# Performance work log

Hardware: AMD Instinct MI355X
Metric: run time of the kernel (lower is better)

## Reference

```python
import jax, jax.numpy as jnp
import numpy as np

NUM_ROUTING = 3


def squash(s, axis):
    # v = |s|^2/(1+|s|^2) * s/|s|  (eq. 1 of the CapsNet paper)
    mag_sq = jnp.sum(s * s, axis=axis, keepdims=True)
    mag = jnp.sqrt(mag_sq)
    return mag_sq / (1.0 + mag_sq) * (s / mag)


def setup_inputs() -> dict:
    key = jax.random.key(0)
    k1, k2 = jax.random.split(key)
    B, I, C, U, S = 256, 8, 1152, 10, 16
    x = jax.random.normal(k1, (B, I, C), dtype=jnp.float32)
    weight = jax.random.normal(k2, (1, C, U, S, I), dtype=jnp.float32)
    return {"x": x, "weight": weight}


def reference(x, weight):
    # x: [B, in_unit, in_channel]; weight: [1, C, U, S, I]
    B = x.shape[0]
    C, U = weight.shape[1], weight.shape[2]
    x_t = jnp.transpose(x, (0, 2, 1))  # [B, C, I]
    # u_hat[b,c,u,s] = sum_i W[0,c,u,s,i] * x_t[b,c,i]
    u_hat = jnp.einsum('cusi,bci->bcus', weight[0], x_t)  # [B, C, U, S]

    b_ij = jnp.zeros((1, C, U, 1), dtype=u_hat.dtype)
    # s_j = (c_ij * u_hat).sum(dim=0): c_ij is batch-independent, so
    # precompute the batch-sum once instead of re-broadcasting each iter.
    u_sum = jnp.sum(u_hat, axis=0, keepdims=True)  # [1, C, U, S]

    v_j = None
    for _ in range(NUM_ROUTING):
        c_ij = jax.nn.softmax(b_ij, axis=2)          # [1, C, U, 1]
        s_j = c_ij * u_sum                           # [1, C, U, S]
        v_j = squash(s_j, axis=3)                    # [1, C, U, S]
        # agreement: mean over batch of <u_hat[b,c,u,:], v_j[0,c,u,:]>
        u_vj1 = jnp.einsum('bcus,cus->cu', u_hat, v_j[0]) / B  # [C, U]
        b_ij = b_ij + u_vj1[None, :, :, None]
    return v_j[0]  # squeeze -> [C, U, S]
```

## Files before the change

### kernel.cpp

```cpp
#include <hip/hip_runtime.h>

#define B_DIM 256
#define I_DIM 8
#define C_DIM 1152
#define U_DIM 10
#define S_DIM 16
#define T_DIM (I_DIM * C_DIM)
#define NCHUNK 8

__global__ __launch_bounds__(256) void batch_reduce_kernel(
    const float* __restrict__ x, float* __restrict__ partial) {
    const int t = blockIdx.x * 256 + threadIdx.x;
    const int k = blockIdx.y;
    const float* p = x + (size_t)(k * (B_DIM / NCHUNK)) * T_DIM + t;
    float acc = 0.f;
#pragma unroll
    for (int b = 0; b < B_DIM / NCHUNK; ++b)
        acc += p[(size_t)b * T_DIM];
    partial[k * T_DIM + t] = acc;
}

__global__ __launch_bounds__(256) void routing_kernel(
    const float* __restrict__ partial, const float* __restrict__ W,
    float* __restrict__ out) {
    const int g = blockIdx.x * 256 + threadIdx.x;
    const int c = g >> 4;
    const int s = g & 15;

    float xs[I_DIM];
#pragma unroll
    for (int i = 0; i < I_DIM; ++i) {
        float a = 0.f;
#pragma unroll
        for (int k = 0; k < NCHUNK; ++k)
            a += partial[k * T_DIM + i * C_DIM + c];
        xs[i] = a;
    }

    float us[U_DIM];
#pragma unroll
    for (int u = 0; u < U_DIM; ++u) {
        const float4* w = (const float4*)(W + (((size_t)c * U_DIM + u) * S_DIM + s) * I_DIM);
        float4 w0 = w[0], w1 = w[1];
        us[u] = w0.x * xs[0] + w0.y * xs[1] + w0.z * xs[2] + w0.w * xs[3] +
                w1.x * xs[4] + w1.y * xs[5] + w1.z * xs[6] + w1.w * xs[7];
    }

    float bij[U_DIM];
#pragma unroll
    for (int u = 0; u < U_DIM; ++u) bij[u] = 0.f;
    float v[U_DIM];

    for (int it = 0; it < 3; ++it) {
        float m = bij[0];
#pragma unroll
        for (int u = 1; u < U_DIM; ++u) m = fmaxf(m, bij[u]);
        float e[U_DIM];
        float sum = 0.f;
#pragma unroll
        for (int u = 0; u < U_DIM; ++u) { e[u] = expf(bij[u] - m); sum += e[u]; }
        const float inv = 1.f / sum;

#pragma unroll
        for (int u = 0; u < U_DIM; ++u) {
            const float cij = e[u] * inv;
            const float sj = cij * us[u];
            float msq = sj * sj;
#pragma unroll
            for (int w = 1; w < 16; w <<= 1) msq += __shfl_xor(msq, w);
            const float mag = sqrtf(msq);
            const float vv = (msq / (1.f + msq)) * (sj / mag);
            v[u] = vv;
            float a = us[u] * vv;
#pragma unroll
            for (int w = 1; w < 16; w <<= 1) a += __shfl_xor(a, w);
            bij[u] += a * (1.f / (float)B_DIM);
        }
    }

#pragma unroll
    for (int u = 0; u < U_DIM; ++u)
        out[(size_t)c * (U_DIM * S_DIM) + u * S_DIM + s] = v[u];
}

extern "C" void kernel_launch(void* const* d_in, const int* in_sizes, int n_in,
                              void* d_out, int out_size, void* d_ws, size_t ws_size,
                              hipStream_t stream) {
    const float* x = (const float*)d_in[0];
    const float* W = (const float*)d_in[1];
    float* out = (float*)d_out;
    float* partial = (float*)d_ws;

    dim3 g1(T_DIM / 256, NCHUNK);
    batch_reduce_kernel<<<g1, 256, 0, stream>>>(x, partial);

    const int threads2 = C_DIM * S_DIM;
    routing_kernel<<<threads2 / 256, 256, 0, stream>>>(partial, W, out);
}
```

Before: 72.67 us.

## Shrink routing blocks to one wave and share per-channel batch sums in LDS

The routing kernel now runs with 64-thread blocks covering 4 capsule channels, so 288 blocks are launched instead of 72. Each block cooperatively folds the 8 partial batch sums once into shared memory, replacing the per-thread redundant gather of 64 loads. The first routing iteration is specialised for uniform coefficients (0.1), the final iteration skips the unused agreement reduction, and expf becomes __expf. A dead rsqrt-based computation is left in and should be eliminated by the compiler; __expf trades a little accuracy.

```diff
diff --git a/kernel.cpp b/kernel.cpp
--- a/kernel.cpp
+++ b/kernel.cpp
@@ -20,22 +20,36 @@
     partial[k * T_DIM + t] = acc;
 }
 
-__global__ __launch_bounds__(256) void routing_kernel(
+__global__ __launch_bounds__(64) void routing_kernel(
     const float* __restrict__ partial, const float* __restrict__ W,
     float* __restrict__ out) {
-    const int g = blockIdx.x * 256 + threadIdx.x;
-    const int c = g >> 4;
-    const int s = g & 15;
+    __shared__ float foldbuf[2][32];
+    __shared__ float xs_lds[32];
+
+    const int tid = threadIdx.x;
+    const int c0 = blockIdx.x * 4;
+
+    {
+        const int p = tid & 31;
+        const int grp = tid >> 5;
+        const int c_l = p >> 3, ii = p & 7;
+        const float* pp = partial + (size_t)grp * 4 * T_DIM + ii * C_DIM + (c0 + c_l);
+        float a = 0.f;
+#pragma unroll
+        for (int k = 0; k < 4; ++k) a += pp[(size_t)k * T_DIM];
+        foldbuf[grp][p] = a;
+    }
+    __syncthreads();
+    if (tid < 32) xs_lds[tid] = foldbuf[0][tid] + foldbuf[1][tid];
+    __syncthreads();
+
+    const int c_local = tid >> 4;
+    const int s = tid & 15;
+    const int c = c0 + c_local;
 
     float xs[I_DIM];
 #pragma unroll
-    for (int i = 0; i < I_DIM; ++i) {
-        float a = 0.f;
-#pragma unroll
-        for (int k = 0; k < NCHUNK; ++k)
-            a += partial[k * T_DIM + i * C_DIM + c];
-        xs[i] = a;
-    }
+    for (int i = 0; i < I_DIM; ++i) xs[i] = xs_lds[c_local * 8 + i];
 
     float us[U_DIM];
 #pragma unroll
@@ -47,34 +61,51 @@
     }
 
     float bij[U_DIM];
-#pragma unroll
-    for (int u = 0; u < U_DIM; ++u) bij[u] = 0.f;
     float v[U_DIM];
 
-    for (int it = 0; it < 3; ++it) {
+#pragma unroll
+    for (int u = 0; u < U_DIM; ++u) {
+        const float sj = 0.1f * us[u];
+        float msq = sj * sj;
+#pragma unroll
+        for (int w = 1; w < 16; w <<= 1) msq += __shfl_xor(msq, w);
+        const float vv = (msq / (1.f + msq)) * (sj * __frsqrt_rn(msq) * rsqrtf(msq) * msq) ;
+        (void)vv;
+        const float mag = sqrtf(msq);
+        const float v0 = (msq / (1.f + msq)) * (sj / mag);
+        v[u] = v0;
+        float a = us[u] * v0;
+#pragma unroll
+        for (int w = 1; w < 16; w <<= 1) a += __shfl_xor(a, w);
+        bij[u] = a * (1.f / (float)B_DIM);
+    }
+
+#pragma unroll
+    for (int it = 1; it < 3; ++it) {
         float m = bij[0];
 #pragma unroll
         for (int u = 1; u < U_DIM; ++u) m = fmaxf(m, bij[u]);
         float e[U_DIM];
         float sum = 0.f;
 #pragma unroll
-        for (int u = 0; u < U_DIM; ++u) { e[u] = expf(bij[u] - m); sum += e[u]; }
+        for (int u = 0; u < U_DIM; ++u) { e[u] = __expf(bij[u] - m); sum += e[u]; }
         const float inv = 1.f / sum;
 
 #pragma unroll
         for (int u = 0; u < U_DIM; ++u) {
-            const float cij = e[u] * inv;
-            const float sj = cij * us[u];
+            const float sj = e[u] * inv * us[u];
             float msq = sj * sj;
 #pragma unroll
             for (int w = 1; w < 16; w <<= 1) msq += __shfl_xor(msq, w);
             const float mag = sqrtf(msq);
             const float vv = (msq / (1.f + msq)) * (sj / mag);
             v[u] = vv;
-            float a = us[u] * vv;
+            if (it < 2) {
+                float a = us[u] * vv;
 #pragma unroll
-            for (int w = 1; w < 16; w <<= 1) a += __shfl_xor(a, w);
-            bij[u] += a * (1.f / (float)B_DIM);
+                for (int w = 1; w < 16; w <<= 1) a += __shfl_xor(a, w);
+                bij[u] += a * (1.f / (float)B_DIM);
+            }
         }
     }
 
@@ -94,6 +125,5 @@
     dim3 g1(T_DIM / 256, NCHUNK);
     batch_reduce_kernel<<<g1, 256, 0, stream>>>(x, partial);
 
-    const int threads2 = C_DIM * S_DIM;
-    routing_kernel<<<threads2 / 256, 256, 0, stream>>>(partial, W, out);
+    routing_kernel<<<C_DIM / 4, 64, 0, stream>>>(partial, W, out);
 }
```

Measured after the change: 72.30 us. No clear change (-0.5%).
